# Kernel optimization log

Hardware: AMD Instinct MI355X
Metric: run time of the kernel (lower is better)

Reference implementation:

```python
import jax, jax.numpy as jnp
import numpy as np

EPS = 1e-8
K_SLOTS, D_SLOT, D_FEAT, D_HID, D_MLP, N_ITER = 8, 256, 768, 256, 256, 3
SCALE = D_HID ** -0.5


def _ln(x, g, b):
    m = jnp.mean(x, axis=-1, keepdims=True)
    v = jnp.var(x, axis=-1, keepdims=True)
    return (x - m) * jax.lax.rsqrt(v + 1e-5) * g + b


def setup_inputs() -> dict:
    key = jax.random.key(0)
    ks = jax.random.split(key, 16)
    s = lambda k, shape, fan: jax.random.normal(k, shape, jnp.float32) * (fan ** -0.5)
    return {
        "features": jax.random.normal(ks[0], (32, 4096, D_FEAT), jnp.float32),
        "prev_slots": jax.random.normal(ks[1], (32, K_SLOTS, D_SLOT), jnp.float32),
        "g_in": jnp.ones((D_FEAT,), jnp.float32), "b_in": jnp.zeros((D_FEAT,), jnp.float32),
        "g_s": jnp.ones((D_SLOT,), jnp.float32), "b_s": jnp.zeros((D_SLOT,), jnp.float32),
        "g_m": jnp.ones((D_SLOT,), jnp.float32), "b_m": jnp.zeros((D_SLOT,), jnp.float32),
        "Wq": s(ks[2], (D_HID, D_SLOT), D_SLOT),
        "Wk": s(ks[3], (D_HID, D_FEAT), D_FEAT),
        "Wv": s(ks[4], (D_SLOT, D_FEAT), D_FEAT),
        "W_ih": s(ks[5], (3 * D_SLOT, D_SLOT), D_SLOT),
        "W_hh": s(ks[6], (3 * D_SLOT, D_SLOT), D_SLOT),
        "b_ih": jnp.zeros((3 * D_SLOT,), jnp.float32),
        "b_hh": jnp.zeros((3 * D_SLOT,), jnp.float32),
        "W1": s(ks[7], (D_MLP, D_SLOT), D_SLOT), "b1": jnp.zeros((D_MLP,), jnp.float32),
        "W2": s(ks[8], (D_SLOT, D_MLP), D_MLP), "b2": jnp.zeros((D_SLOT,), jnp.float32),
    }


def reference(features, prev_slots, g_in, b_in, g_s, b_s, g_m, b_m,
              Wq, Wk, Wv, W_ih, W_hh, b_ih, b_hh, W1, b1, W2, b2):
    # features: (B, N, D_feat); prev_slots: (B, K, D_slot)
    fn = _ln(features, g_in, b_in)
    k = jnp.einsum('bnf,hf->bnh', fn, Wk)   # (B, N, H)
    v = jnp.einsum('bnf,df->bnd', fn, Wv)   # (B, N, D_slot)

    def attn_of(slots):
        q = jnp.einsum('bkd,hd->bkh', _ln(slots, g_s, b_s), Wq)
        logits = jnp.einsum('bkh,bnh->bkn', q, k) * SCALE
        return jax.nn.softmax(logits, axis=1)  # softmax over slot axis K

    slots = prev_slots
    for _ in range(N_ITER):
        attn = attn_of(slots)
        attn_n = attn / (jnp.sum(attn, axis=-1, keepdims=True) + EPS)
        updates = jnp.einsum('bkn,bnd->bkd', attn_n, v)
        # torch GRUCell (gates ordered r, z, n)
        gi = jnp.einsum('bkd,gd->bkg', updates, W_ih) + b_ih
        gh = jnp.einsum('bkd,gd->bkg', slots, W_hh) + b_hh
        gi_r, gi_z, gi_n = jnp.split(gi, 3, axis=-1)
        gh_r, gh_z, gh_n = jnp.split(gh, 3, axis=-1)
        r = jax.nn.sigmoid(gi_r + gh_r)
        z = jax.nn.sigmoid(gi_z + gh_z)
        n = jnp.tanh(gi_n + r * gh_n)
        h = (1.0 - z) * n + z * slots
        mlp = jnp.einsum('bkm,dm->bkd',
                         jax.nn.relu(jnp.einsum('bkd,md->bkm', _ln(h, g_m, b_m), W1) + b1),
                         W2) + b2
        slots = h + mlp

    attn_final = attn_of(slots)  # (B, K, N)
    # TTT3R confidence-weighted blend with previous slots
    mask = jax.nn.sigmoid(jnp.mean(attn_final, axis=-1))[..., None]  # (B, K, 1)
    slots_out = slots * mask + prev_slots * (1.0 - mask)
    return slots_out, attn_final
```

## Files before the change

### kernel.cpp

```cpp
#include <hip/hip_runtime.h>

typedef unsigned int uint;
typedef unsigned short ushort;
typedef __bf16 bf16x8 __attribute__((ext_vector_type(8)));
typedef float f32x4 __attribute__((ext_vector_type(4)));

#define B_SZ 32
#define N_SEQ 4096
#define ROWS (B_SZ * N_SEQ)
#define LN_EPS 1e-5f
#define EPS_SUM 1e-8f
#define QSCALE 0.0625f

__device__ inline float u2f(uint x){ union{uint u; float f;} c; c.u = x; return c.f; }
__device__ inline ushort f2bf(float f){
  union{float f; uint u;} c; c.f = f; uint u = c.u;
  return (ushort)((u + 0x7fffu + ((u >> 16) & 1u)) >> 16);
}
__device__ inline uint pack2(float a, float b){ return (uint)f2bf(a) | ((uint)f2bf(b) << 16); }
__device__ inline void unpk8(uint4 u, float* o){
  o[0]=u2f(u.x<<16); o[1]=u2f(u.x&0xffff0000u);
  o[2]=u2f(u.y<<16); o[3]=u2f(u.y&0xffff0000u);
  o[4]=u2f(u.z<<16); o[5]=u2f(u.z&0xffff0000u);
  o[6]=u2f(u.w<<16); o[7]=u2f(u.w&0xffff0000u);
}
__device__ inline f32x4 mfma16(bf16x8 a, bf16x8 b, f32x4 c){
  return __builtin_amdgcn_mfma_f32_16x16x32_bf16(a, b, c, 0, 0, 0);
}

__global__ __launch_bounds__(256) void prep_kernel(
    const float* Wk, const float* Wv, const float* g_in, const float* b_in,
    const float* W_ih, const float* W_hh, const float* W1, const float* W2, const float* Wq,
    const float* prev_slots,
    ushort* Wg, ushort* Wihb, ushort* Whhb, ushort* W1b, ushort* W2b, ushort* Wqb,
    float* wb, float* wg, float* slots, ushort* qb)
{
  __shared__ float ra[4], rb[4];
  int blk = blockIdx.x, t = threadIdx.x;
  if (blk < 1536){
    int idx = blk*256 + t;
    int o = idx / 768, f = idx - o*768;
    float w = (o < 256) ? Wk[o*768 + f] : Wv[(o-256)*768 + f];
    Wg[idx] = f2bf(w * g_in[f]);
  } else if (blk < 2304){
    int idx = (blk-1536)*256 + t; Wihb[idx] = f2bf(W_ih[idx]);
  } else if (blk < 3072){
    int idx = (blk-2304)*256 + t; Whhb[idx] = f2bf(W_hh[idx]);
  } else if (blk < 3328){
    int idx = (blk-3072)*256 + t; W1b[idx] = f2bf(W1[idx]);
  } else if (blk < 3584){
    int idx = (blk-3328)*256 + t; W2b[idx] = f2bf(W2[idx]);
  } else if (blk < 3840){
    int idx = (blk-3584)*256 + t; Wqb[idx] = f2bf(Wq[idx]);
  } else if (blk < 4352){
    int o = blk - 3840;
    float ab = 0.f, ag = 0.f;
    for (int i = 0; i < 3; ++i){
      int f = t + 256*i;
      float w = (o < 256) ? Wk[o*768 + f] : Wv[(o-256)*768 + f];
      ab += w * b_in[f]; ag += w * g_in[f];
    }
    int lane = t & 63, wv = t >> 6;
    for (int off = 1; off < 64; off <<= 1){ ab += __shfl_xor(ab, off); ag += __shfl_xor(ag, off); }
    if (lane == 0){ ra[wv] = ab; rb[wv] = ag; }
    __syncthreads();
    if (t == 0){ wb[o] = ra[0]+ra[1]+ra[2]+ra[3]; wg[o] = rb[0]+rb[1]+rb[2]+rb[3]; }
  } else if (blk < 4608){
    int idx = (blk-4352)*256 + t; slots[idx] = prev_slots[idx];
  } else {
    int idx = (blk-4608)*256 + t;
    int b = idx >> 11, rem = idx & 2047, rr = rem >> 8, d = rem & 255;
    qb[b*4096 + (8+rr)*256 + d] = 0;
  }
}

__global__ __launch_bounds__(256) void stats_kernel(const float* feat, float* meanv, float* rstdv){
  int t = threadIdx.x, w = t >> 6, lane = t & 63;
  int row = blockIdx.x*4 + w;
  const float4* fp = (const float4*)(feat + (size_t)row * 768);
  float s = 0.f, q = 0.f;
  for (int i = 0; i < 3; ++i){
    float4 v = fp[lane + 64*i];
    s += v.x + v.y + v.z + v.w;
    q += v.x*v.x + v.y*v.y + v.z*v.z + v.w*v.w;
  }
  for (int off = 1; off < 64; off <<= 1){ s += __shfl_xor(s, off); q += __shfl_xor(q, off); }
  if (lane == 0){
    float m = s * (1.f/768.f);
    meanv[row] = m;
    rstdv[row] = rsqrtf(q * (1.f/768.f) - m*m + LN_EPS);
  }
}

__global__ __launch_bounds__(256, 2) void kv_gemm(
    const float* feat, const ushort* Wg, const float* wb, const float* wg,
    const float* meanv, const float* rstdv, ushort* kv)
{
  int blk = blockIdx.x; int r0 = blk * 64;
  int t = threadIdx.x, w = t >> 6, lane = t & 63, m16 = lane & 15, quad = lane >> 4;
  __shared__ __align__(16) uint As[64*20];
  __shared__ __align__(16) uint Bs[512*20];
  __shared__ float mr_m[64], mr_r[64], wbl[512], wgl[512];
  if (t < 64){ mr_m[t] = meanv[r0 + t]; mr_r[t] = rstdv[r0 + t]; }
  wbl[t] = wb[t]; wbl[t+256] = wb[t+256];
  wgl[t] = wg[t]; wgl[t+256] = wg[t+256];

  f32x4 acc[4][8];
  #pragma unroll
  for (int i = 0; i < 4; ++i)
    #pragma unroll
    for (int j = 0; j < 8; ++j) acc[i][j] = (f32x4){0.f,0.f,0.f,0.f};

  for (int k0 = 0; k0 < 768; k0 += 32){
    __syncthreads();
    #pragma unroll
    for (int i = 0; i < 2; ++i){
      int c = t + 256*i;
      int row = c >> 3, f4i = c & 7;
      float4 v = *(const float4*)(feat + (size_t)(r0+row)*768 + k0 + f4i*4);
      uint2 pk; pk.x = pack2(v.x, v.y); pk.y = pack2(v.z, v.w);
      *(uint2*)&As[row*20 + f4i*2] = pk;
    }
    #pragma unroll
    for (int i = 0; i < 8; ++i){
      int c = t + 256*i;
      int o = c >> 2, ko = c & 3;
      uint4 wv = *(const uint4*)(Wg + (size_t)o*768 + k0 + ko*8);
      *(uint4*)&Bs[o*20 + ko*4] = wv;
    }
    __syncthreads();
    bf16x8 af[4];
    #pragma unroll
    for (int i = 0; i < 4; ++i)
      af[i] = __builtin_bit_cast(bf16x8, *(const uint4*)&As[(16*i + m16)*20 + quad*4]);
    #pragma unroll
    for (int j = 0; j < 8; ++j){
      bf16x8 bfv = __builtin_bit_cast(bf16x8, *(const uint4*)&Bs[(w*128 + 16*j + m16)*20 + quad*4]);
      #pragma unroll
      for (int i = 0; i < 4; ++i) acc[i][j] = mfma16(af[i], bfv, acc[i][j]);
    }
  }
  #pragma unroll
  for (int i = 0; i < 4; ++i){
    #pragma unroll
    for (int j = 0; j < 8; ++j){
      int col = w*128 + 16*j + m16;
      float wgc = wgl[col], wbc = wbl[col];
      f32x4 c = acc[i][j];
      #pragma unroll
      for (int r = 0; r < 4; ++r){
        int row = 16*i + quad*4 + r;
        float val = mr_r[row] * (c[r] - mr_m[row]*wgc) + wbc;
        kv[(size_t)(r0+row)*512 + col] = f2bf(val);
      }
    }
  }
}

__global__ __launch_bounds__(256) void q_kernel(
    const float* slots, const ushort* Wqb, const float* g_s, const float* b_s, ushort* qb)
{
  int blk = blockIdx.x; int b = blk >> 3, kk = blk & 7;
  int t = threadIdx.x, lane = t & 63, w = t >> 6;
  __shared__ __align__(16) float ln_l[256];
  __shared__ float ra[4], rb[4];
  float x = slots[blk*256 + t];
  float s = x, q = x*x;
  for (int off = 1; off < 64; off <<= 1){ s += __shfl_xor(s, off); q += __shfl_xor(q, off); }
  if (lane == 0){ ra[w] = s; rb[w] = q; }
  __syncthreads();
  float S = ra[0]+ra[1]+ra[2]+ra[3], Q = rb[0]+rb[1]+rb[2]+rb[3];
  float mean = S * (1.f/256.f);
  float rstd = rsqrtf(Q * (1.f/256.f) - mean*mean + LN_EPS);
  ln_l[t] = (x - mean)*rstd*g_s[t] + b_s[t];
  __syncthreads();
  float acc = 0.f;
  const uint4* wq = (const uint4*)(Wqb + (size_t)t*256);
  for (int c = 0; c < 32; ++c){
    float wf[8]; unpk8(wq[c], wf);
    const float* lp = &ln_l[c*8];
    #pragma unroll
    for (int j = 0; j < 8; ++j) acc += wf[j]*lp[j];
  }
  qb[(size_t)(b*16 + kk)*256 + t] = f2bf(acc * QSCALE);
}

__global__ __launch_bounds__(256) void attn_kernel(
    const ushort* kv, const ushort* qb,
    float* upd_part, float* sum_part, float* attn_out, int mode)
{
  int chunk = blockIdx.x, b = blockIdx.y;
  int t = threadIdx.x, w = t >> 6, lane = t & 63, m16 = lane & 15, quad = lane >> 4;
  int n0 = chunk * 256;
  __shared__ __align__(16) float PT[256*9];
  __shared__ float wsum[4][8];
  __shared__ __align__(16) float red[8*2048];

  bf16x8 af[8];
  {
    const uint4* qp = (const uint4*)(qb + ((size_t)(b*16 + m16))*256);
    #pragma unroll
    for (int ks = 0; ks < 8; ++ks) af[ks] = __builtin_bit_cast(bf16x8, qp[ks*4 + quad]);
  }
  const ushort* kvb = kv + ((size_t)(b*4096 + n0))*512;
  f32x4 acc[4];
  #pragma unroll
  for (int nf = 0; nf < 4; ++nf) acc[nf] = (f32x4){0.f,0.f,0.f,0.f};
  #pragma unroll
  for (int ks = 0; ks < 8; ++ks){
    #pragma unroll
    for (int nf = 0; nf < 4; ++nf){
      const uint4* bp = (const uint4*)(kvb + ((size_t)(w*64 + nf*16 + m16))*512);
      bf16x8 bv = __builtin_bit_cast(bf16x8, bp[ks*4 + quad]);
      acc[nf] = mfma16(af[ks], bv, acc[nf]);
    }
  }
  float sacc[4] = {0.f,0.f,0.f,0.f};
  #pragma unroll
  for (int nf = 0; nf < 4; ++nf){
    float l0 = acc[nf][0], l1 = acc[nf][1], l2 = acc[nf][2], l3 = acc[nf][3];
    float mx = fmaxf(fmaxf(l0,l1), fmaxf(l2,l3));
    mx = fmaxf(mx, __shfl_xor(mx, 16));
    float e0 = __expf(l0-mx), e1 = __expf(l1-mx), e2 = __expf(l2-mx), e3 = __expf(l3-mx);
    float s = e0+e1+e2+e3;
    s += __shfl_xor(s, 16);
    float inv = 1.f / s;
    e0 *= inv; e1 *= inv; e2 *= inv; e3 *= inv;
    if (quad < 2){
      sacc[0]+=e0; sacc[1]+=e1; sacc[2]+=e2; sacc[3]+=e3;
      int pos = w*64 + nf*16 + m16;
      if (mode == 0){
        PT[pos*9 + quad*4 + 0] = e0;
        PT[pos*9 + quad*4 + 1] = e1;
        PT[pos*9 + quad*4 + 2] = e2;
        PT[pos*9 + quad*4 + 3] = e3;
      } else {
        int slot = quad*4;
        attn_out[((size_t)(b*8 + slot+0))*4096 + n0 + pos] = e0;
        attn_out[((size_t)(b*8 + slot+1))*4096 + n0 + pos] = e1;
        attn_out[((size_t)(b*8 + slot+2))*4096 + n0 + pos] = e2;
        attn_out[((size_t)(b*8 + slot+3))*4096 + n0 + pos] = e3;
      }
    }
  }
  for (int off = 1; off < 16; off <<= 1){
    sacc[0] += __shfl_xor(sacc[0], off);
    sacc[1] += __shfl_xor(sacc[1], off);
    sacc[2] += __shfl_xor(sacc[2], off);
    sacc[3] += __shfl_xor(sacc[3], off);
  }
  if (m16 == 0 && quad < 2){
    wsum[w][quad*4+0] = sacc[0]; wsum[w][quad*4+1] = sacc[1];
    wsum[w][quad*4+2] = sacc[2]; wsum[w][quad*4+3] = sacc[3];
  }
  __syncthreads();
  if (t < 8){
    float s = wsum[0][t] + wsum[1][t] + wsum[2][t] + wsum[3][t];
    sum_part[(b*16 + chunk)*8 + t] = s;
  }
  if (mode) return;
  int dg = t & 31, pg = t >> 5;
  float ua[8][8];
  #pragma unroll
  for (int k = 0; k < 8; ++k)
    #pragma unroll
    for (int j = 0; j < 8; ++j) ua[k][j] = 0.f;
  const ushort* vb = kv + ((size_t)(b*4096 + n0))*512 + 256;
  for (int i = 0; i < 32; ++i){
    int p = pg*32 + i;
    uint4 vv = *(const uint4*)(vb + (size_t)p*512 + dg*8);
    float vf[8]; unpk8(vv, vf);
    #pragma unroll
    for (int k = 0; k < 8; ++k){
      float a = PT[p*9 + k];
      #pragma unroll
      for (int j = 0; j < 8; ++j) ua[k][j] += a * vf[j];
    }
  }
  #pragma unroll
  for (int k = 0; k < 8; ++k){
    *(float4*)&red[pg*2048 + k*256 + dg*8]     = make_float4(ua[k][0],ua[k][1],ua[k][2],ua[k][3]);
    *(float4*)&red[pg*2048 + k*256 + dg*8 + 4] = make_float4(ua[k][4],ua[k][5],ua[k][6],ua[k][7]);
  }
  __syncthreads();
  #pragma unroll
  for (int j = 0; j < 8; ++j){
    float s = 0.f;
    #pragma unroll
    for (int pgi = 0; pgi < 8; ++pgi) s += red[pgi*2048 + j*256 + t];
    upd_part[((size_t)((b*16 + chunk)*8 + j))*256 + t] = s;
  }
}

__global__ __launch_bounds__(256) void gru_kernel(
    const float* upd_part, const float* sum_part, float* slots,
    const ushort* Wihb, const ushort* Whhb, const ushort* W1b, const ushort* W2b,
    const float* b_ih, const float* b_hh, const float* g_m, const float* b_m,
    const float* b1, const float* b2)
{
  int blk = blockIdx.x; int b = blk >> 3, k = blk & 7;
  int t = threadIdx.x, lane = t & 63, w = t >> 6;
  __shared__ __align__(16) float u_l[256], s_l[256], lnh[256], m1_l[256];
  __shared__ float ra[4], rb[4];
  float stot = EPS_SUM;
  for (int c = 0; c < 16; ++c) stot += sum_part[(b*16 + c)*8 + k];
  float us = 0.f;
  for (int c = 0; c < 16; ++c) us += upd_part[((size_t)((b*16 + c)*8 + k))*256 + t];
  u_l[t] = us / stot;
  s_l[t] = slots[blk*256 + t];
  __syncthreads();
  float gi[3], gh[3];
  for (int gg = 0; gg < 3; ++gg){
    int g = gg*256 + t;
    float ai = b_ih[g], ah = b_hh[g];
    const uint4* wi = (const uint4*)(Wihb + (size_t)g*256);
    const uint4* wh = (const uint4*)(Whhb + (size_t)g*256);
    for (int c = 0; c < 32; ++c){
      float wf[8], hf[8];
      unpk8(wi[c], wf); unpk8(wh[c], hf);
      const float* up = &u_l[c*8];
      const float* sp = &s_l[c*8];
      #pragma unroll
      for (int j = 0; j < 8; ++j){ ai += wf[j]*up[j]; ah += hf[j]*sp[j]; }
    }
    gi[gg] = ai; gh[gg] = ah;
  }
  float r = 1.f/(1.f + __expf(-(gi[0] + gh[0])));
  float z = 1.f/(1.f + __expf(-(gi[1] + gh[1])));
  float n = tanhf(gi[2] + r*gh[2]);
  float h = (1.f - z)*n + z*s_l[t];
  float s = h, q = h*h;
  for (int off = 1; off < 64; off <<= 1){ s += __shfl_xor(s, off); q += __shfl_xor(q, off); }
  if (lane == 0){ ra[w] = s; rb[w] = q; }
  __syncthreads();
  float S = ra[0]+ra[1]+ra[2]+ra[3], Q = rb[0]+rb[1]+rb[2]+rb[3];
  float mean = S * (1.f/256.f);
  float rstd = rsqrtf(Q * (1.f/256.f) - mean*mean + LN_EPS);
  lnh[t] = (h - mean)*rstd*g_m[t] + b_m[t];
  __syncthreads();
  float a1 = b1[t];
  {
    const uint4* w1 = (const uint4*)(W1b + (size_t)t*256);
    for (int c = 0; c < 32; ++c){
      float wf[8]; unpk8(w1[c], wf);
      const float* lp = &lnh[c*8];
      #pragma unroll
      for (int j = 0; j < 8; ++j) a1 += wf[j]*lp[j];
    }
  }
  m1_l[t] = fmaxf(a1, 0.f);
  __syncthreads();
  float a2 = b2[t];
  {
    const uint4* w2 = (const uint4*)(W2b + (size_t)t*256);
    for (int c = 0; c < 32; ++c){
      float wf[8]; unpk8(w2[c], wf);
      const float* mp = &m1_l[c*8];
      #pragma unroll
      for (int j = 0; j < 8; ++j) a2 += wf[j]*mp[j];
    }
  }
  slots[blk*256 + t] = h + a2;
}

__global__ __launch_bounds__(256) void blend_kernel(
    const float* slots, const float* prev, const float* sum_part, float* out)
{
  int blk = blockIdx.x; int b = blk >> 3, k = blk & 7;
  int t = threadIdx.x;
  float s = 0.f;
  for (int c = 0; c < 16; ++c) s += sum_part[(b*16 + c)*8 + k];
  float mean = s * (1.f/4096.f);
  float mask = 1.f/(1.f + __expf(-mean));
  int idx = blk*256 + t;
  out[idx] = slots[idx]*mask + prev[idx]*(1.f - mask);
}

extern "C" void kernel_launch(void* const* d_in, const int* in_sizes, int n_in,
                              void* d_out, int out_size, void* d_ws, size_t ws_size,
                              hipStream_t stream)
{
  (void)in_sizes; (void)n_in; (void)out_size; (void)ws_size;
  const float* feat = (const float*)d_in[0];
  const float* prev = (const float*)d_in[1];
  const float* g_in = (const float*)d_in[2];
  const float* b_in = (const float*)d_in[3];
  const float* g_s  = (const float*)d_in[4];
  const float* b_s  = (const float*)d_in[5];
  const float* g_m  = (const float*)d_in[6];
  const float* b_m  = (const float*)d_in[7];
  const float* Wq   = (const float*)d_in[8];
  const float* Wk   = (const float*)d_in[9];
  const float* Wv   = (const float*)d_in[10];
  const float* W_ih = (const float*)d_in[11];
  const float* W_hh = (const float*)d_in[12];
  const float* b_ih = (const float*)d_in[13];
  const float* b_hh = (const float*)d_in[14];
  const float* W1   = (const float*)d_in[15];
  const float* b1   = (const float*)d_in[16];
  const float* W2   = (const float*)d_in[17];
  const float* b2   = (const float*)d_in[18];
  float* out = (float*)d_out;

  char* ws = (char*)d_ws;
  size_t off = 0;
  auto alloc = [&](size_t bytes)->void*{
    void* p = ws + off;
    off = (off + bytes + 255) & ~(size_t)255;
    return p;
  };
  ushort* kv    = (ushort*)alloc((size_t)ROWS*512*2);
  ushort* Wg    = (ushort*)alloc((size_t)512*768*2);
  float*  wbv   = (float*) alloc(512*4);
  float*  wgv   = (float*) alloc(512*4);
  float*  meanv = (float*) alloc((size_t)ROWS*4);
  float*  rstdv = (float*) alloc((size_t)ROWS*4);
  ushort* Wihb  = (ushort*)alloc((size_t)768*256*2);
  ushort* Whhb  = (ushort*)alloc((size_t)768*256*2);
  ushort* W1b   = (ushort*)alloc((size_t)256*256*2);
  ushort* W2b   = (ushort*)alloc((size_t)256*256*2);
  ushort* Wqb   = (ushort*)alloc((size_t)256*256*2);
  float*  slots = (float*) alloc((size_t)65536*4);
  ushort* qb    = (ushort*)alloc((size_t)32*16*256*2);
  float*  updp  = (float*) alloc((size_t)32*16*8*256*4);
  float*  sump  = (float*) alloc((size_t)32*16*8*4);

  prep_kernel<<<4864, 256, 0, stream>>>(Wk, Wv, g_in, b_in, W_ih, W_hh, W1, W2, Wq, prev,
      Wg, Wihb, Whhb, W1b, W2b, Wqb, wbv, wgv, slots, qb);
  stats_kernel<<<ROWS/4, 256, 0, stream>>>(feat, meanv, rstdv);
  kv_gemm<<<ROWS/64, 256, 0, stream>>>(feat, Wg, wbv, wgv, meanv, rstdv, kv);

  float* attn_out = out + 65536;
  for (int it = 0; it < 3; ++it){
    q_kernel<<<256, 256, 0, stream>>>(slots, Wqb, g_s, b_s, qb);
    attn_kernel<<<dim3(16, 32), 256, 0, stream>>>(kv, qb, updp, sump, attn_out, 0);
    gru_kernel<<<256, 256, 0, stream>>>(updp, sump, slots, Wihb, Whhb, W1b, W2b,
        b_ih, b_hh, g_m, b_m, b1, b2);
  }
  q_kernel<<<256, 256, 0, stream>>>(slots, Wqb, g_s, b_s, qb);
  attn_kernel<<<dim3(16, 32), 256, 0, stream>>>(kv, qb, updp, sump, attn_out, 1);
  blend_kernel<<<256, 256, 0, stream>>>(slots, prev, sump, out);
}
```

Baseline: 1.015 ms.

## Pre-convert features to bf16 and retile KV GEMM with direct-to-LDS loads

The stats pass now also writes a bf16 copy of the features. The KV GEMM reads that copy and switches from a 64-row by 512-column tile to a 128x128 tile on a 2D grid. Tiles go straight into LDS via global_load_lds with an XOR swizzle, and K steps are 64 wide. This halves the GEMM's feature read bandwidth and removes the in-loop fp32 packing, at the cost of an extra bf16 feature write and read round trip through memory, plus four column blocks each re-reading the same rows.

```diff
diff --git a/kernel.cpp b/kernel.cpp
--- a/kernel.cpp
+++ b/kernel.cpp
@@ -26,6 +26,11 @@
 }
 __device__ inline f32x4 mfma16(bf16x8 a, bf16x8 b, f32x4 c){
   return __builtin_amdgcn_mfma_f32_16x16x32_bf16(a, b, c, 0, 0, 0);
+}
+typedef const __attribute__((address_space(1))) void ga_void;
+typedef __attribute__((address_space(3))) void ls_void;
+__device__ inline void gll16(const void* g, void* l){
+  __builtin_amdgcn_global_load_lds((ga_void*)g, (ls_void*)l, 16, 0, 0);
 }
 
 __global__ __launch_bounds__(256) void prep_kernel(
@@ -74,15 +79,21 @@
   }
 }
 
-__global__ __launch_bounds__(256) void stats_kernel(const float* feat, float* meanv, float* rstdv){
+__global__ __launch_bounds__(256) void cvt_stats_kernel(
+    const float* feat, ushort* featb, float* meanv, float* rstdv)
+{
   int t = threadIdx.x, w = t >> 6, lane = t & 63;
   int row = blockIdx.x*4 + w;
   const float4* fp = (const float4*)(feat + (size_t)row * 768);
+  uint2* ob = (uint2*)(featb + (size_t)row * 768);
   float s = 0.f, q = 0.f;
+  #pragma unroll
   for (int i = 0; i < 3; ++i){
     float4 v = fp[lane + 64*i];
     s += v.x + v.y + v.z + v.w;
     q += v.x*v.x + v.y*v.y + v.z*v.z + v.w*v.w;
+    uint2 pk; pk.x = pack2(v.x, v.y); pk.y = pack2(v.z, v.w);
+    ob[lane + 64*i] = pk;
   }
   for (int off = 1; off < 64; off <<= 1){ s += __shfl_xor(s, off); q += __shfl_xor(q, off); }
   if (lane == 0){
@@ -92,66 +103,82 @@
   }
 }
 
-__global__ __launch_bounds__(256, 2) void kv_gemm(
-    const float* feat, const ushort* Wg, const float* wb, const float* wg,
+__global__ __launch_bounds__(256) void kv_gemm(
+    const ushort* featb, const ushort* Wg, const float* wb, const float* wg,
     const float* meanv, const float* rstdv, ushort* kv)
 {
-  int blk = blockIdx.x; int r0 = blk * 64;
+  int r0 = blockIdx.x * 128, c0 = blockIdx.y * 128;
   int t = threadIdx.x, w = t >> 6, lane = t & 63, m16 = lane & 15, quad = lane >> 4;
-  __shared__ __align__(16) uint As[64*20];
-  __shared__ __align__(16) uint Bs[512*20];
-  __shared__ float mr_m[64], mr_r[64], wbl[512], wgl[512];
-  if (t < 64){ mr_m[t] = meanv[r0 + t]; mr_r[t] = rstdv[r0 + t]; }
-  wbl[t] = wb[t]; wbl[t+256] = wb[t+256];
-  wgl[t] = wg[t]; wgl[t+256] = wg[t+256];
-
-  f32x4 acc[4][8];
+  __shared__ __align__(16) ushort As[128*64];
+  __shared__ __align__(16) ushort Bs[128*64];
+  __shared__ float mr_m[128], mr_r[128], wbl[128], wgl[128];
+  if (t < 128){
+    mr_m[t] = meanv[r0 + t]; mr_r[t] = rstdv[r0 + t];
+    wbl[t] = wb[c0 + t];     wgl[t] = wg[c0 + t];
+  }
+  int wr = (w >> 1) * 64, wc = (w & 1) * 64;
+  int srow = t >> 3, skc = t & 7;
+
+  f32x4 acc[4][4];
   #pragma unroll
   for (int i = 0; i < 4; ++i)
     #pragma unroll
-    for (int j = 0; j < 8; ++j) acc[i][j] = (f32x4){0.f,0.f,0.f,0.f};
-
-  for (int k0 = 0; k0 < 768; k0 += 32){
+    for (int j = 0; j < 4; ++j) acc[i][j] = (f32x4){0.f,0.f,0.f,0.f};
+
+  for (int k0 = 0; k0 < 768; k0 += 64){
+    if (k0) __syncthreads();
+    #pragma unroll
+    for (int i = 0; i < 4; ++i){
+      int row = srow + i*32;
+      int kcg = skc ^ (row & 7);
+      gll16(featb + (size_t)(r0+row)*768 + k0 + kcg*8, As + (i*256 + w*64)*8);
+    }
+    #pragma unroll
+    for (int i = 0; i < 4; ++i){
+      int col = srow + i*32;
+      int kcg = skc ^ (col & 7);
+      gll16(Wg + (size_t)(c0+col)*768 + k0 + kcg*8, Bs + (i*256 + w*64)*8);
+    }
     __syncthreads();
-    #pragma unroll
-    for (int i = 0; i < 2; ++i){
-      int c = t + 256*i;
-      int row = c >> 3, f4i = c & 7;
-      float4 v = *(const float4*)(feat + (size_t)(r0+row)*768 + k0 + f4i*4);
-      uint2 pk; pk.x = pack2(v.x, v.y); pk.y = pack2(v.z, v.w);
-      *(uint2*)&As[row*20 + f4i*2] = pk;
-    }
-    #pragma unroll
-    for (int i = 0; i < 8; ++i){
-      int c = t + 256*i;
-      int o = c >> 2, ko = c & 3;
-      uint4 wv = *(const uint4*)(Wg + (size_t)o*768 + k0 + ko*8);
-      *(uint4*)&Bs[o*20 + ko*4] = wv;
-    }
-    __syncthreads();
-    bf16x8 af[4];
-    #pragma unroll
-    for (int i = 0; i < 4; ++i)
-      af[i] = __builtin_bit_cast(bf16x8, *(const uint4*)&As[(16*i + m16)*20 + quad*4]);
-    #pragma unroll
-    for (int j = 0; j < 8; ++j){
-      bf16x8 bfv = __builtin_bit_cast(bf16x8, *(const uint4*)&Bs[(w*128 + 16*j + m16)*20 + quad*4]);
-      #pragma unroll
-      for (int i = 0; i < 4; ++i) acc[i][j] = mfma16(af[i], bfv, acc[i][j]);
-    }
+    bf16x8 af[4][2], bfr[4][2];
+    #pragma unroll
+    for (int i = 0; i < 4; ++i){
+      int row = wr + 16*i + m16;
+      #pragma unroll
+      for (int h = 0; h < 2; ++h){
+        int kc = (quad + h*4) ^ (row & 7);
+        af[i][h] = __builtin_bit_cast(bf16x8, *(const uint4*)&As[(row*8 + kc)*8]);
+      }
+    }
+    #pragma unroll
+    for (int j = 0; j < 4; ++j){
+      int col = wc + 16*j + m16;
+      #pragma unroll
+      for (int h = 0; h < 2; ++h){
+        int kc = (quad + h*4) ^ (col & 7);
+        bfr[j][h] = __builtin_bit_cast(bf16x8, *(const uint4*)&Bs[(col*8 + kc)*8]);
+      }
+    }
+    #pragma unroll
+    for (int j = 0; j < 4; ++j)
+      #pragma unroll
+      for (int i = 0; i < 4; ++i){
+        acc[i][j] = mfma16(af[i][0], bfr[j][0], acc[i][j]);
+        acc[i][j] = mfma16(af[i][1], bfr[j][1], acc[i][j]);
+      }
   }
   #pragma unroll
   for (int i = 0; i < 4; ++i){
     #pragma unroll
-    for (int j = 0; j < 8; ++j){
-      int col = w*128 + 16*j + m16;
+    for (int j = 0; j < 4; ++j){
+      int col = wc + 16*j + m16;
       float wgc = wgl[col], wbc = wbl[col];
       f32x4 c = acc[i][j];
       #pragma unroll
       for (int r = 0; r < 4; ++r){
-        int row = 16*i + quad*4 + r;
+        int row = wr + 16*i + quad*4 + r;
         float val = mr_r[row] * (c[r] - mr_m[row]*wgc) + wbc;
-        kv[(size_t)(r0+row)*512 + col] = f2bf(val);
+        kv[(size_t)(r0+row)*512 + c0 + col] = f2bf(val);
       }
     }
   }
@@ -410,6 +437,7 @@
     return p;
   };
   ushort* kv    = (ushort*)alloc((size_t)ROWS*512*2);
+  ushort* featb = (ushort*)alloc((size_t)ROWS*768*2);
   ushort* Wg    = (ushort*)alloc((size_t)512*768*2);
   float*  wbv   = (float*) alloc(512*4);
   float*  wgv   = (float*) alloc(512*4);
@@ -427,8 +455,8 @@
 
   prep_kernel<<<4864, 256, 0, stream>>>(Wk, Wv, g_in, b_in, W_ih, W_hh, W1, W2, Wq, prev,
       Wg, Wihb, Whhb, W1b, W2b, Wqb, wbv, wgv, slots, qb);
-  stats_kernel<<<ROWS/4, 256, 0, stream>>>(feat, meanv, rstdv);
-  kv_gemm<<<ROWS/64, 256, 0, stream>>>(feat, Wg, wbv, wgv, meanv, rstdv, kv);
+  cvt_stats_kernel<<<ROWS/4, 256, 0, stream>>>(feat, featb, meanv, rstdv);
+  kv_gemm<<<dim3(ROWS/128, 4), 256, 0, stream>>>(featb, Wg, wbv, wgv, meanv, rstdv, kv);
 
   float* attn_out = out + 65536;
   for (int it = 0; it < 3; ++it){
```

Measured after the change: 972.8 us. 1.04x faster.
